# Kernel tuning notes

Hardware: AMD Instinct MI355X
Metric: run time of the kernel (lower is better)

Reference implementation:

```python
import jax, jax.numpy as jnp
import numpy as np

B, C, H, W = 2, 256, 48, 48
NUM_HEADS = 8
HEAD_DIM = C // NUM_HEADS
SCALE = HEAD_DIM ** (-0.5)


def setup_inputs() -> dict:
    key = jax.random.key(0)
    ks = jax.random.split(key, 5)
    s = 1.0 / np.sqrt(C)  # conv1x1 fan-in scaling
    return {
        "x": jax.random.normal(ks[0], (B, C, H, W), jnp.float32),
        "Wq": jax.random.normal(ks[1], (C, C), jnp.float32) * s,
        "bq": jnp.zeros((C,), jnp.float32),
        "Wk": jax.random.normal(ks[2], (C, C), jnp.float32) * s,
        "bk": jnp.zeros((C,), jnp.float32),
        "Wv": jax.random.normal(ks[3], (C, C), jnp.float32) * s,
        "bv": jnp.zeros((C,), jnp.float32),
        "Wo": jax.random.normal(ks[4], (C, C), jnp.float32) * s,
        "bo": jnp.zeros((C,), jnp.float32),
    }


def _proj(x, Wf, bf):
    # conv1x1: [B,C,H,W] x [Cout,Cin] -> [B,Cout,H,W]
    return jnp.einsum('bchw,oc->bohw', x, Wf) + bf[None, :, None, None]


def reference(x, Wq, bq, Wk, bk, Wv, bv, Wo, bo):
    b, c, h, w = x.shape
    n = h * w
    # projections then split heads: [B, heads, N, head_dim]
    def to_heads(t):
        return t.reshape(b, NUM_HEADS, HEAD_DIM, n).transpose(0, 1, 3, 2)
    q = to_heads(_proj(x, Wq, bq))
    k = to_heads(_proj(x, Wk, bk))
    v = to_heads(_proj(x, Wv, bv))
    attn = jnp.einsum('bhnd,bhmd->bhnm', q, k) * SCALE
    attn = jax.nn.softmax(attn, axis=-1)  # max-subtract + softmax (stable)
    out = jnp.einsum('bhnm,bhmd->bhnd', attn, v)
    out = out.transpose(0, 1, 3, 2).reshape(b, c, h, w)
    return _proj(out, Wo, bo)
```

## Files before the change

### kernel.cpp

```cpp
#include <hip/hip_runtime.h>
#include <hip/hip_bf16.h>

#define BATCH 2
#define CH 256
#define NH 8
#define HD 32
#define NPOS 2304
#define SCALE 0.17677669529663687f
#define QSCALE 0.25503482f
#define NSPLIT 3
#define KSPAN (NPOS / NSPLIT)
#define NT (KSPAN / 128)
#define QT (NPOS / 16)

typedef __attribute__((ext_vector_type(8))) short short8;
typedef __attribute__((ext_vector_type(4))) short short4e;
typedef __attribute__((ext_vector_type(4))) float f32x4;
typedef __attribute__((ext_vector_type(4))) unsigned int u32x4;
typedef __attribute__((ext_vector_type(2))) unsigned int u32x2;

__device__ __forceinline__ unsigned short f2bf(float f) {
    unsigned int u = __builtin_bit_cast(unsigned int, f);
    u += 0x7FFFu + ((u >> 16) & 1u);
    return (unsigned short)(u >> 16);
}

__device__ __forceinline__ unsigned int cvt_pk_bf16(float a, float b) {
    unsigned int r;
    asm("v_cvt_pk_bf16_f32 %0, %1, %2" : "=v"(r) : "v"(a), "v"(b));
    return r;
}

__device__ __forceinline__ float fast_exp2(float x) {
    float r;
    asm("v_exp_f32 %0, %1" : "=v"(r) : "v"(x));
    return r;
}

#define GLOAD_LDS16(gsrc, ldst) \
    __builtin_amdgcn_global_load_lds( \
        (const __attribute__((address_space(1))) void*)(gsrc), \
        (__attribute__((address_space(3))) void*)(ldst), 16, 0, 0)

__global__ __launch_bounds__(256) void prep(
    const float* __restrict__ Wq, const float* __restrict__ Wk,
    const float* __restrict__ Wv, const float* __restrict__ Wo,
    const float* __restrict__ x,
    unsigned short* __restrict__ wbf, unsigned short* __restrict__ xT)
{
    __shared__ float Ts[32][33];
    int id = blockIdx.x;
    int t = threadIdx.x;
    if (id < 256) {
        int which = id >> 6;
        const float* src = (which == 0) ? Wq : (which == 1) ? Wk : (which == 2) ? Wv : Wo;
        unsigned short* d = wbf + (size_t)which * CH * CH;
        int i = ((id & 63) * 256 + t) * 4;
        f32x4 v = *(const f32x4*)&src[i];
        short4e o;
        #pragma unroll
        for (int j = 0; j < 4; ++j) o[j] = (short)f2bf(v[j]);
        *(short4e*)&d[i] = o;
    } else {
        int tid = id - 256;
        int b = tid / 576;
        int rem = tid % 576;
        int c0 = (rem / 72) * 32;
        int n0 = (rem % 72) * 32;
        int col = t & 31, row = t >> 5;
        #pragma unroll
        for (int i = 0; i < 4; ++i)
            Ts[row + i * 8][col] = x[((size_t)b * CH + c0 + row + i * 8) * NPOS + n0 + col];
        __syncthreads();
        #pragma unroll
        for (int i = 0; i < 4; ++i)
            xT[((size_t)b * NPOS + n0 + row + i * 8) * CH + c0 + col] = f2bf(Ts[col][row + i * 8]);
    }
}

__global__ __launch_bounds__(256) void qkv_gemm(
    const unsigned short* __restrict__ xT,
    const unsigned short* __restrict__ Wb,
    const float* __restrict__ bq, const float* __restrict__ bk,
    const float* __restrict__ bv,
    unsigned short* __restrict__ qout, unsigned short* __restrict__ kout,
    unsigned short* __restrict__ vout)
{
    int b = blockIdx.z;
    int n0 = blockIdx.x * 64;
    int o0 = blockIdx.y * 32;
    int t = threadIdx.x, w = t >> 6, lane = t & 63;
    int lo = lane & 15, hi = lane >> 4;
    int ob = o0 + (w & 1) * 16;
    int nb = n0 + (w >> 1) * 32;

    const unsigned short* Wq = Wb;
    const unsigned short* Wk = Wb + (size_t)CH * CH;
    const unsigned short* Wv = Wb + (size_t)2 * CH * CH;
    const unsigned short* xb = xT + ((size_t)b * NPOS + nb) * CH;

    f32x4 aq[2] = {}, ak[2] = {}, av[2] = {};

    for (int k0 = 0; k0 < CH; k0 += 32) {
        short8 wqf = *(const short8*)&Wq[(size_t)(ob + lo) * CH + k0 + hi * 8];
        short8 wkf = *(const short8*)&Wk[(size_t)(ob + lo) * CH + k0 + hi * 8];
        short8 wvf = *(const short8*)&Wv[(size_t)(ob + lo) * CH + k0 + hi * 8];
        #pragma unroll
        for (int g = 0; g < 2; ++g) {
            short8 xf = *(const short8*)&xb[(size_t)(g * 16 + lo) * CH + k0 + hi * 8];
            aq[g] = __builtin_amdgcn_mfma_f32_16x16x32_bf16(wqf, xf, aq[g], 0, 0, 0);
            ak[g] = __builtin_amdgcn_mfma_f32_16x16x32_bf16(wkf, xf, ak[g], 0, 0, 0);
            av[g] = __builtin_amdgcn_mfma_f32_16x16x32_bf16(wvf, xf, av[g], 0, 0, 0);
        }
    }

    int h = ob >> 5;
    int olow = (ob & 31) + hi * 4;
    int rr = lo & 3, qd = lo >> 2;
    #pragma unroll
    for (int g = 0; g < 2; ++g) {
        int n = nb + g * 16 + lo;
        size_t qkbase = ((size_t)(b * NH + h) * NPOS + n) * HD + olow;
        short4e pq, pk;
        #pragma unroll
        for (int r = 0; r < 4; ++r) {
            int o = ob + hi * 4 + r;
            pq[r] = (short)f2bf((aq[g][r] + bq[o]) * QSCALE);
            pk[r] = (short)f2bf(ak[g][r] + bk[o]);
        }
        *(short4e*)&qout[qkbase] = pq;
        *(short4e*)&kout[qkbase] = pk;

        float v0 = av[g][0] + bv[ob + hi * 4 + 0];
        float v1 = av[g][1] + bv[ob + hi * 4 + 1];
        float v2 = av[g][2] + bv[ob + hi * 4 + 2];
        float v3 = av[g][3] + bv[ob + hi * 4 + 3];
        float p, r_;
        p = (rr & 1) ? v0 : v1; r_ = __shfl_xor(p, 1); if (rr & 1) v0 = r_; else v1 = r_;
        p = (rr & 1) ? v2 : v3; r_ = __shfl_xor(p, 1); if (rr & 1) v2 = r_; else v3 = r_;
        p = (rr & 2) ? v0 : v2; r_ = __shfl_xor(p, 2); if (rr & 2) v0 = r_; else v2 = r_;
        p = (rr & 2) ? v1 : v3; r_ = __shfl_xor(p, 2); if (rr & 2) v1 = r_; else v3 = r_;
        u32x2 pr;
        pr[0] = cvt_pk_bf16(v0, v1);
        pr[1] = cvt_pk_bf16(v2, v3);
        int nbase = nb + g * 16;
        int G = (nbase & 127) >> 4;
        int pbase;
        if (G < 4) {
            pbase = G * 32 + qd * 8;
        } else {
            int gam = G & 3;
            pbase = (qd >= 2) ? (gam * 32 + (qd - 2) * 8 + 4)
                              : ((gam ^ 1) * 32 + (qd + 2) * 8 + 4);
        }
        int d = (ob & 31) + hi * 4 + rr;
        size_t vaddr = ((size_t)(b * NH + h) * HD + d) * NPOS + (nbase & ~127) + pbase;
        *(u32x2*)&vout[vaddr] = pr;
    }
}

__global__ __launch_bounds__(256) void attn_split(
    const unsigned short* __restrict__ Q,
    const unsigned short* __restrict__ K,
    const unsigned short* __restrict__ V,
    float* __restrict__ Opart,
    float* __restrict__ Lpart)
{
    const int N = NPOS;
    int xb_ = blockIdx.x;
    int bh = xb_ & 15;
    int split = xb_ >> 4;
    int w = threadIdx.x >> 6;
    int qt = blockIdx.y * 4 + w;
    int n0 = qt * 16;
    int lane = threadIdx.x & 63;
    int lo = lane & 15, hi = lane >> 4;
    bool upperhalf = lane >= 32;

    __shared__ unsigned short Ks[2][128 * HD];
    __shared__ unsigned short Vs[2][HD * 128];

    short8 qa = *(const short8*)(Q + ((size_t)bh * N + n0 + lo) * HD + hi * 8);

    const unsigned short* Kb = K + (size_t)bh * N * HD;
    const unsigned short* Vb = V + (size_t)bh * HD * N;

    short8 ones;
    #pragma unroll
    for (int j = 0; j < 8; ++j) ones[j] = (short)0x3F80;

    f32x4 oacc[2] = {{0.f,0.f,0.f,0.f},{0.f,0.f,0.f,0.f}};
    f32x4 lacc = {0.f,0.f,0.f,0.f};

    const int kbeg = split * KSPAN;

    auto stage = [&](int bidx, int k0) {
        #pragma unroll
        for (int j = 0; j < 2; ++j) {
            int L = w * 128 + j * 64 + lane;
            int row = L >> 2, blk = L & 3;
            const unsigned short* src = Kb + (size_t)(k0 + row) * HD + (blk ^ (row & 3)) * 8;
            GLOAD_LDS16(src, &Ks[bidx][(size_t)(w * 128 + j * 64) * 8]);
        }
        #pragma unroll
        for (int j = 0; j < 2; ++j) {
            int L = w * 128 + j * 64 + lane;
            int row = L >> 4, blk = L & 15;
            const unsigned short* src = Vb + (size_t)row * N + k0 + (blk ^ (row & 15)) * 8;
            GLOAD_LDS16(src, &Vs[bidx][(size_t)(w * 128 + j * 64) * 8]);
        }
    };

    stage(0, kbeg);
    __syncthreads();

    int buf = 0;
    #pragma unroll
    for (int kt = 0; kt < NT; ++kt) {
        int k0 = kbeg + kt * 128;
        if (kt + 1 < NT) stage(buf ^ 1, k0 + 128);

        f32x4 s[8];
        __builtin_amdgcn_s_setprio(1);
        #pragma unroll
        for (int g = 0; g < 8; ++g) {
            short8 kf = *(const short8*)&Ks[buf][(g * 16 + lo) * HD + (hi ^ (lo & 3)) * 8];
            s[g] = __builtin_amdgcn_mfma_f32_16x16x32_bf16(kf, qa, (f32x4){0.f,0.f,0.f,0.f}, 0, 0, 0);
        }
        __builtin_amdgcn_s_setprio(0);

        #pragma unroll
        for (int g = 0; g < 8; ++g)
            #pragma unroll
            for (int r = 0; r < 4; ++r)
                s[g][r] = fast_exp2(s[g][r]);

        unsigned int pk0[8], pk1[8];
        #pragma unroll
        for (int g = 0; g < 8; ++g) {
            pk0[g] = cvt_pk_bf16(s[g][0], s[g][1]);
            pk1[g] = cvt_pk_bf16(s[g][2], s[g][3]);
        }

        __builtin_amdgcn_s_setprio(1);
        #pragma unroll
        for (int c = 0; c < 4; ++c) {
            unsigned int z0 = upperhalf ? pk0[4 + c] : pk0[4 + (c ^ 1)];
            unsigned int z1 = upperhalf ? pk1[4 + c] : pk1[4 + (c ^ 1)];
            unsigned int r0 = (unsigned int)__shfl_xor((int)z0, 32);
            unsigned int r1 = (unsigned int)__shfl_xor((int)z1, 32);
            u32x4 fv = {pk0[c], pk1[c], r0, r1};
            short8 frag = __builtin_bit_cast(short8, fv);

            lacc = __builtin_amdgcn_mfma_f32_16x16x32_bf16(frag, ones, lacc, 0, 0, 0);
            #pragma unroll
            for (int df = 0; df < 2; ++df) {
                short8 vf = *(const short8*)&Vs[buf][(df * 16 + lo) * 128 + ((c * 4 + hi) ^ lo) * 8];
                oacc[df] = __builtin_amdgcn_mfma_f32_16x16x32_bf16(frag, vf, oacc[df], 0, 0, 0);
            }
        }
        __builtin_amdgcn_s_setprio(0);

        __syncthreads();
        buf ^= 1;
    }

    size_t tidx  = (((size_t)bh * QT + qt) * NSPLIT + split);
    float* ob = Opart + tidx * (HD * 16);
    #pragma unroll
    for (int df = 0; df < 2; ++df)
        *(f32x4*)&ob[(df * 16 + lo) * 16 + hi * 4] = oacc[df];
    if (lo == 0) {
        float* lb = Lpart + tidx * 16;
        #pragma unroll
        for (int r = 0; r < 4; ++r) lb[hi * 4 + r] = lacc[r];
    }
}

__global__ __launch_bounds__(256) void attn_merge(
    const float* __restrict__ Opart,
    const float* __restrict__ Lpart,
    unsigned short* __restrict__ omT)
{
    int bh = blockIdx.y, b = bh >> 3, h = bh & 7;
    int qt = blockIdx.x, n0 = qt * 16;
    int t = threadIdx.x;
    int d = t & 31;
    int r0 = t >> 5;
    size_t base = ((size_t)bh * QT + qt) * NSPLIT;
    #pragma unroll
    for (int i = 0; i < 2; ++i) {
        int row = r0 + i * 8;
        float osum = 0.f, lsum = 0.f;
        #pragma unroll
        for (int s = 0; s < NSPLIT; ++s) {
            osum += Opart[(base + s) * (HD * 16) + d * 16 + row];
            lsum += Lpart[(base + s) * 16 + row];
        }
        omT[((size_t)b * NPOS + n0 + row) * CH + h * HD + d] = f2bf(osum / lsum);
    }
}

__global__ __launch_bounds__(256) void wo_gemm(
    const unsigned short* __restrict__ omT,
    const unsigned short* __restrict__ Wo,
    const float* __restrict__ bo,
    float* __restrict__ out)
{
    int b = blockIdx.z;
    int n0 = blockIdx.x * 64;
    int o0 = blockIdx.y * 32;
    int t = threadIdx.x, w = t >> 6, lane = t & 63;
    int lo = lane & 15, hi = lane >> 4;
    int ob = o0 + (w & 1) * 16;
    int nb = n0 + (w >> 1) * 32;

    const unsigned short* xb = omT + ((size_t)b * NPOS + nb) * CH;

    f32x4 acc[2] = {};
    for (int k0 = 0; k0 < CH; k0 += 32) {
        short8 wf = *(const short8*)&Wo[(size_t)(ob + lo) * CH + k0 + hi * 8];
        #pragma unroll
        for (int g = 0; g < 2; ++g) {
            short8 xf = *(const short8*)&xb[(size_t)(g * 16 + lo) * CH + k0 + hi * 8];
            acc[g] = __builtin_amdgcn_mfma_f32_16x16x32_bf16(wf, xf, acc[g], 0, 0, 0);
        }
    }

    #pragma unroll
    for (int g = 0; g < 2; ++g) {
        int n = nb + g * 16 + lo;
        #pragma unroll
        for (int r = 0; r < 4; ++r) {
            int o = ob + hi * 4 + r;
            out[((size_t)b * CH + o) * NPOS + n] = acc[g][r] + bo[o];
        }
    }
}

extern "C" void kernel_launch(void* const* d_in, const int* in_sizes, int n_in,
                              void* d_out, int out_size, void* d_ws, size_t ws_size,
                              hipStream_t stream) {
    const float* x  = (const float*)d_in[0];
    const float* Wq = (const float*)d_in[1];
    const float* bq = (const float*)d_in[2];
    const float* Wk = (const float*)d_in[3];
    const float* bk = (const float*)d_in[4];
    const float* Wv = (const float*)d_in[5];
    const float* bv = (const float*)d_in[6];
    const float* Wo = (const float*)d_in[7];
    const float* bo = (const float*)d_in[8];
    float* out = (float*)d_out;

    const size_t E  = (size_t)BATCH * CH * NPOS;
    const size_t WS = (size_t)CH * CH;
    unsigned short* wbf = (unsigned short*)d_ws;
    unsigned short* xT  = wbf + 4 * WS;
    unsigned short* qb  = xT + E;
    unsigned short* kb  = qb + E;
    unsigned short* vT  = kb + E;
    float* Opart = (float*)(vT + E);
    float* Lpart = Opart + (size_t)16 * QT * NSPLIT * (HD * 16);
    unsigned short* om = xT;
    (void)ws_size; (void)in_sizes; (void)n_in; (void)out_size;

    hipLaunchKernelGGL(prep, dim3(256 + 1152), dim3(256), 0, stream,
                       Wq, Wk, Wv, Wo, x, wbf, xT);
    hipLaunchKernelGGL(qkv_gemm, dim3(NPOS / 64, CH / 32, BATCH), dim3(256), 0, stream,
                       xT, wbf, bq, bk, bv, qb, kb, vT);
    hipLaunchKernelGGL(attn_split, dim3(NSPLIT * 16, QT / 4), dim3(256), 0, stream,
                       qb, kb, vT, Opart, Lpart);
    hipLaunchKernelGGL(attn_merge, dim3(QT, BATCH * NH), dim3(256), 0, stream,
                       Opart, Lpart, om);
    hipLaunchKernelGGL(wo_gemm, dim3(NPOS / 64, CH / 32, BATCH), dim3(256), 0, stream,
                       om, wbf + 3 * WS, bo, out);
}
```

Baseline: 71.74 us.

## Process two query tiles per wavefront in split attention to reuse K/V fragments

```diff
diff --git a/kernel.cpp b/kernel.cpp
--- a/kernel.cpp
+++ b/kernel.cpp
@@ -171,8 +171,8 @@
     int bh = xb_ & 15;
     int split = xb_ >> 4;
     int w = threadIdx.x >> 6;
-    int qt = blockIdx.y * 4 + w;
-    int n0 = qt * 16;
+    int qtA = blockIdx.y * 8 + w * 2;
+    int qtB = qtA + 1;
     int lane = threadIdx.x & 63;
     int lo = lane & 15, hi = lane >> 4;
     bool upperhalf = lane >= 32;
@@ -180,7 +180,8 @@
     __shared__ unsigned short Ks[2][128 * HD];
     __shared__ unsigned short Vs[2][HD * 128];
 
-    short8 qa = *(const short8*)(Q + ((size_t)bh * N + n0 + lo) * HD + hi * 8);
+    short8 qaA = *(const short8*)(Q + ((size_t)bh * N + qtA * 16 + lo) * HD + hi * 8);
+    short8 qaB = *(const short8*)(Q + ((size_t)bh * N + qtB * 16 + lo) * HD + hi * 8);
 
     const unsigned short* Kb = K + (size_t)bh * N * HD;
     const unsigned short* Vb = V + (size_t)bh * HD * N;
@@ -189,8 +190,10 @@
     #pragma unroll
     for (int j = 0; j < 8; ++j) ones[j] = (short)0x3F80;
 
-    f32x4 oacc[2] = {{0.f,0.f,0.f,0.f},{0.f,0.f,0.f,0.f}};
-    f32x4 lacc = {0.f,0.f,0.f,0.f};
+    f32x4 oaccA[2] = {{0.f,0.f,0.f,0.f},{0.f,0.f,0.f,0.f}};
+    f32x4 oaccB[2] = {{0.f,0.f,0.f,0.f},{0.f,0.f,0.f,0.f}};
+    f32x4 laccA = {0.f,0.f,0.f,0.f};
+    f32x4 laccB = {0.f,0.f,0.f,0.f};
 
     const int kbeg = split * KSPAN;
 
@@ -220,44 +223,57 @@
         int k0 = kbeg + kt * 128;
         if (kt + 1 < NT) stage(buf ^ 1, k0 + 128);
 
-        f32x4 s[8];
+        f32x4 sA[8], sB[8];
         __builtin_amdgcn_s_setprio(1);
         #pragma unroll
         for (int g = 0; g < 8; ++g) {
             short8 kf = *(const short8*)&Ks[buf][(g * 16 + lo) * HD + (hi ^ (lo & 3)) * 8];
-            s[g] = __builtin_amdgcn_mfma_f32_16x16x32_bf16(kf, qa, (f32x4){0.f,0.f,0.f,0.f}, 0, 0, 0);
+            sA[g] = __builtin_amdgcn_mfma_f32_16x16x32_bf16(kf, qaA, (f32x4){0.f,0.f,0.f,0.f}, 0, 0, 0);
+            sB[g] = __builtin_amdgcn_mfma_f32_16x16x32_bf16(kf, qaB, (f32x4){0.f,0.f,0.f,0.f}, 0, 0, 0);
         }
         __builtin_amdgcn_s_setprio(0);
 
-        #pragma unroll
-        for (int g = 0; g < 8; ++g)
+        unsigned int pkA0[8], pkA1[8], pkB0[8], pkB1[8];
+        #pragma unroll
+        for (int g = 0; g < 8; ++g) {
             #pragma unroll
-            for (int r = 0; r < 4; ++r)
-                s[g][r] = fast_exp2(s[g][r]);
-
-        unsigned int pk0[8], pk1[8];
+            for (int r = 0; r < 4; ++r) sA[g][r] = fast_exp2(sA[g][r]);
+            pkA0[g] = cvt_pk_bf16(sA[g][0], sA[g][1]);
+            pkA1[g] = cvt_pk_bf16(sA[g][2], sA[g][3]);
+        }
         #pragma unroll
         for (int g = 0; g < 8; ++g) {
-            pk0[g] = cvt_pk_bf16(s[g][0], s[g][1]);
-            pk1[g] = cvt_pk_bf16(s[g][2], s[g][3]);
+            #pragma unroll
+            for (int r = 0; r < 4; ++r) sB[g][r] = fast_exp2(sB[g][r]);
+            pkB0[g] = cvt_pk_bf16(sB[g][0], sB[g][1]);
+            pkB1[g] = cvt_pk_bf16(sB[g][2], sB[g][3]);
         }
 
         __builtin_amdgcn_s_setprio(1);
         #pragma unroll
         for (int c = 0; c < 4; ++c) {
-            unsigned int z0 = upperhalf ? pk0[4 + c] : pk0[4 + (c ^ 1)];
-            unsigned int z1 = upperhalf ? pk1[4 + c] : pk1[4 + (c ^ 1)];
-            unsigned int r0 = (unsigned int)__shfl_xor((int)z0, 32);
-            unsigned int r1 = (unsigned int)__shfl_xor((int)z1, 32);
-            u32x4 fv = {pk0[c], pk1[c], r0, r1};
-            short8 frag = __builtin_bit_cast(short8, fv);
-
-            lacc = __builtin_amdgcn_mfma_f32_16x16x32_bf16(frag, ones, lacc, 0, 0, 0);
-            #pragma unroll
-            for (int df = 0; df < 2; ++df) {
-                short8 vf = *(const short8*)&Vs[buf][(df * 16 + lo) * 128 + ((c * 4 + hi) ^ lo) * 8];
-                oacc[df] = __builtin_amdgcn_mfma_f32_16x16x32_bf16(frag, vf, oacc[df], 0, 0, 0);
-            }
+            unsigned int zA0 = upperhalf ? pkA0[4 + c] : pkA0[4 + (c ^ 1)];
+            unsigned int zA1 = upperhalf ? pkA1[4 + c] : pkA1[4 + (c ^ 1)];
+            unsigned int zB0 = upperhalf ? pkB0[4 + c] : pkB0[4 + (c ^ 1)];
+            unsigned int zB1 = upperhalf ? pkB1[4 + c] : pkB1[4 + (c ^ 1)];
+            unsigned int rA0 = (unsigned int)__shfl_xor((int)zA0, 32);
+            unsigned int rA1 = (unsigned int)__shfl_xor((int)zA1, 32);
+            unsigned int rB0 = (unsigned int)__shfl_xor((int)zB0, 32);
+            unsigned int rB1 = (unsigned int)__shfl_xor((int)zB1, 32);
+            u32x4 fvA = {pkA0[c], pkA1[c], rA0, rA1};
+            u32x4 fvB = {pkB0[c], pkB1[c], rB0, rB1};
+            short8 fragA = __builtin_bit_cast(short8, fvA);
+            short8 fragB = __builtin_bit_cast(short8, fvB);
+
+            short8 vf0 = *(const short8*)&Vs[buf][(0 * 16 + lo) * 128 + ((c * 4 + hi) ^ lo) * 8];
+            short8 vf1 = *(const short8*)&Vs[buf][(1 * 16 + lo) * 128 + ((c * 4 + hi) ^ lo) * 8];
+
+            laccA = __builtin_amdgcn_mfma_f32_16x16x32_bf16(fragA, ones, laccA, 0, 0, 0);
+            laccB = __builtin_amdgcn_mfma_f32_16x16x32_bf16(fragB, ones, laccB, 0, 0, 0);
+            oaccA[0] = __builtin_amdgcn_mfma_f32_16x16x32_bf16(fragA, vf0, oaccA[0], 0, 0, 0);
+            oaccA[1] = __builtin_amdgcn_mfma_f32_16x16x32_bf16(fragA, vf1, oaccA[1], 0, 0, 0);
+            oaccB[0] = __builtin_amdgcn_mfma_f32_16x16x32_bf16(fragB, vf0, oaccB[0], 0, 0, 0);
+            oaccB[1] = __builtin_amdgcn_mfma_f32_16x16x32_bf16(fragB, vf1, oaccB[1], 0, 0, 0);
         }
         __builtin_amdgcn_s_setprio(0);
 
@@ -265,15 +281,29 @@
         buf ^= 1;
     }
 
-    size_t tidx  = (((size_t)bh * QT + qt) * NSPLIT + split);
-    float* ob = Opart + tidx * (HD * 16);
-    #pragma unroll
-    for (int df = 0; df < 2; ++df)
-        *(f32x4*)&ob[(df * 16 + lo) * 16 + hi * 4] = oacc[df];
-    if (lo == 0) {
-        float* lb = Lpart + tidx * 16;
-        #pragma unroll
-        for (int r = 0; r < 4; ++r) lb[hi * 4 + r] = lacc[r];
+    {
+        size_t tidx = (((size_t)bh * QT + qtA) * NSPLIT + split);
+        float* ob = Opart + tidx * (HD * 16);
+        #pragma unroll
+        for (int df = 0; df < 2; ++df)
+            *(f32x4*)&ob[(df * 16 + lo) * 16 + hi * 4] = oaccA[df];
+        if (lo == 0) {
+            float* lb = Lpart + tidx * 16;
+            #pragma unroll
+            for (int r = 0; r < 4; ++r) lb[hi * 4 + r] = laccA[r];
+        }
+    }
+    {
+        size_t tidx = (((size_t)bh * QT + qtB) * NSPLIT + split);
+        float* ob = Opart + tidx * (HD * 16);
+        #pragma unroll
+        for (int df = 0; df < 2; ++df)
+            *(f32x4*)&ob[(df * 16 + lo) * 16 + hi * 4] = oaccB[df];
+        if (lo == 0) {
+            float* lb = Lpart + tidx * 16;
+            #pragma unroll
+            for (int r = 0; r < 4; ++r) lb[hi * 4 + r] = laccB[r];
+        }
     }
 }
 
@@ -368,7 +398,7 @@
                        Wq, Wk, Wv, Wo, x, wbf, xT);
     hipLaunchKernelGGL(qkv_gemm, dim3(NPOS / 64, CH / 32, BATCH), dim3(256), 0, stream,
                        xT, wbf, bq, bk, bv, qb, kb, vT);
-    hipLaunchKernelGGL(attn_split, dim3(NSPLIT * 16, QT / 4), dim3(256), 0, stream,
+    hipLaunchKernelGGL(attn_split, dim3(NSPLIT * 16, QT / 8), dim3(256), 0, stream,
                        qb, kb, vT, Opart, Lpart);
     hipLaunchKernelGGL(attn_merge, dim3(QT, BATCH * NH), dim3(256), 0, stream,
                        Opart, Lpart, om);
```

Measured after the change: 72.68 us. Within noise of the previous version (+1.3%).

## Fuse split-attention merge into output projection GEMM via shared memory

Applied to the files above, without the earlier changes.

```diff
diff --git a/kernel.cpp b/kernel.cpp
--- a/kernel.cpp
+++ b/kernel.cpp
@@ -12,6 +12,7 @@
 #define KSPAN (NPOS / NSPLIT)
 #define NT (KSPAN / 128)
 #define QT (NPOS / 16)
+#define OMPAD 264
 
 typedef __attribute__((ext_vector_type(8))) short short8;
 typedef __attribute__((ext_vector_type(4))) short short4e;
@@ -277,63 +278,69 @@
     }
 }
 
-__global__ __launch_bounds__(256) void attn_merge(
+__global__ __launch_bounds__(256) void merge_wo(
     const float* __restrict__ Opart,
     const float* __restrict__ Lpart,
-    unsigned short* __restrict__ omT)
-{
-    int bh = blockIdx.y, b = bh >> 3, h = bh & 7;
-    int qt = blockIdx.x, n0 = qt * 16;
-    int t = threadIdx.x;
-    int d = t & 31;
-    int r0 = t >> 5;
-    size_t base = ((size_t)bh * QT + qt) * NSPLIT;
-    #pragma unroll
-    for (int i = 0; i < 2; ++i) {
-        int row = r0 + i * 8;
-        float osum = 0.f, lsum = 0.f;
-        #pragma unroll
-        for (int s = 0; s < NSPLIT; ++s) {
-            osum += Opart[(base + s) * (HD * 16) + d * 16 + row];
-            lsum += Lpart[(base + s) * 16 + row];
-        }
-        omT[((size_t)b * NPOS + n0 + row) * CH + h * HD + d] = f2bf(osum / lsum);
-    }
-}
-
-__global__ __launch_bounds__(256) void wo_gemm(
-    const unsigned short* __restrict__ omT,
     const unsigned short* __restrict__ Wo,
     const float* __restrict__ bo,
     float* __restrict__ out)
 {
-    int b = blockIdx.z;
-    int n0 = blockIdx.x * 64;
-    int o0 = blockIdx.y * 32;
-    int t = threadIdx.x, w = t >> 6, lane = t & 63;
+    int qt = blockIdx.x;
+    int b  = blockIdx.y;
+    int t = threadIdx.x;
+
+    __shared__ unsigned short omL[16 * OMPAD];
+
+    {
+        int c = t;
+        int h = c >> 5, d = c & 31;
+        size_t tbase = (((size_t)(b * NH + h) * QT + qt) * NSPLIT);
+        float osum[16];
+        #pragma unroll
+        for (int j = 0; j < 4; ++j) {
+            f32x4 a0 = *(const f32x4*)&Opart[(tbase + 0) * (HD * 16) + d * 16 + j * 4];
+            f32x4 a1 = *(const f32x4*)&Opart[(tbase + 1) * (HD * 16) + d * 16 + j * 4];
+            f32x4 a2 = *(const f32x4*)&Opart[(tbase + 2) * (HD * 16) + d * 16 + j * 4];
+            #pragma unroll
+            for (int r = 0; r < 4; ++r) osum[j * 4 + r] = a0[r] + a1[r] + a2[r];
+        }
+        float linv[16];
+        #pragma unroll
+        for (int j = 0; j < 4; ++j) {
+            f32x4 l0 = *(const f32x4*)&Lpart[(tbase + 0) * 16 + j * 4];
+            f32x4 l1 = *(const f32x4*)&Lpart[(tbase + 1) * 16 + j * 4];
+            f32x4 l2 = *(const f32x4*)&Lpart[(tbase + 2) * 16 + j * 4];
+            #pragma unroll
+            for (int r = 0; r < 4; ++r) linv[j * 4 + r] = 1.f / (l0[r] + l1[r] + l2[r]);
+        }
+        #pragma unroll
+        for (int r = 0; r < 16; ++r)
+            omL[r * OMPAD + c] = f2bf(osum[r] * linv[r]);
+    }
+    __syncthreads();
+
+    int w = t >> 6, lane = t & 63;
     int lo = lane & 15, hi = lane >> 4;
-    int ob = o0 + (w & 1) * 16;
-    int nb = n0 + (w >> 1) * 32;
-
-    const unsigned short* xb = omT + ((size_t)b * NPOS + nb) * CH;
-
-    f32x4 acc[2] = {};
+    int ow = w * 64;
+
+    f32x4 acc[4] = {};
+    #pragma unroll
     for (int k0 = 0; k0 < CH; k0 += 32) {
-        short8 wf = *(const short8*)&Wo[(size_t)(ob + lo) * CH + k0 + hi * 8];
-        #pragma unroll
-        for (int g = 0; g < 2; ++g) {
-            short8 xf = *(const short8*)&xb[(size_t)(g * 16 + lo) * CH + k0 + hi * 8];
-            acc[g] = __builtin_amdgcn_mfma_f32_16x16x32_bf16(wf, xf, acc[g], 0, 0, 0);
-        }
-    }
-
-    #pragma unroll
-    for (int g = 0; g < 2; ++g) {
-        int n = nb + g * 16 + lo;
+        short8 bfr = *(const short8*)&omL[lo * OMPAD + k0 + hi * 8];
+        #pragma unroll
+        for (int f = 0; f < 4; ++f) {
+            short8 wf = *(const short8*)&Wo[(size_t)(ow + f * 16 + lo) * CH + k0 + hi * 8];
+            acc[f] = __builtin_amdgcn_mfma_f32_16x16x32_bf16(wf, bfr, acc[f], 0, 0, 0);
+        }
+    }
+
+    int n = qt * 16 + lo;
+    #pragma unroll
+    for (int f = 0; f < 4; ++f) {
         #pragma unroll
         for (int r = 0; r < 4; ++r) {
-            int o = ob + hi * 4 + r;
-            out[((size_t)b * CH + o) * NPOS + n] = acc[g][r] + bo[o];
+            int o = ow + f * 16 + hi * 4 + r;
+            out[((size_t)b * CH + o) * NPOS + n] = acc[f][r] + bo[o];
         }
     }
 }
@@ -361,7 +368,6 @@
     unsigned short* vT  = kb + E;
     float* Opart = (float*)(vT + E);
     float* Lpart = Opart + (size_t)16 * QT * NSPLIT * (HD * 16);
-    unsigned short* om = xT;
     (void)ws_size; (void)in_sizes; (void)n_in; (void)out_size;
 
     hipLaunchKernelGGL(prep, dim3(256 + 1152), dim3(256), 0, stream,
@@ -370,8 +376,6 @@
                        xT, wbf, bq, bk, bv, qb, kb, vT);
     hipLaunchKernelGGL(attn_split, dim3(NSPLIT * 16, QT / 4), dim3(256), 0, stream,
                        qb, kb, vT, Opart, Lpart);
-    hipLaunchKernelGGL(attn_merge, dim3(QT, BATCH * NH), dim3(256), 0, stream,
-                       Opart, Lpart, om);
-    hipLaunchKernelGGL(wo_gemm, dim3(NPOS / 64, CH / 32, BATCH), dim3(256), 0, stream,
-                       om, wbf + 3 * WS, bo, out);
-}
+    hipLaunchKernelGGL(merge_wo, dim3(QT, BATCH), dim3(256), 0, stream,
+                       Opart, Lpart, wbf + 3 * WS, bo, out);
+}
```

Result: faster. 64.48 us (median of 2 runs) (-10.1%).
